# Kernel tuning notes

Measured on AMD Instinct MI355X. Metric: run time of the kernel, lower is better.

## Reference

```python
import jax, jax.numpy as jnp
import numpy as np

DIM = 256
HEADS = 8
PS = 8  # patch/window size
EPS = 1e-5


def _ln(x, g, b):
    m = x.mean(-1, keepdims=True)
    v = x.var(-1, keepdims=True)
    return (x - m) / jnp.sqrt(v + EPS) * g + b


def setup_inputs() -> dict:
    key = jax.random.key(0)
    ks = jax.random.split(key, 10)
    B, C, H, W = 4, DIM, 256, 256
    s = 0.02
    return {
        "y_lf": jax.random.normal(ks[0], (B, C, H, W), jnp.float32),
        "y_hf": jax.random.normal(ks[1], (B, C, H, W), jnp.float32),
        "g_lf": jnp.ones((C,), jnp.float32),
        "b_lf": jnp.zeros((C,), jnp.float32),
        "g_hf": jnp.ones((C,), jnp.float32),
        "b_hf": jnp.zeros((C,), jnp.float32),
        "Wq": jax.random.normal(ks[2], (C, C), jnp.float32) * s,
        "bq": jnp.zeros((C,), jnp.float32),
        "Wk": jax.random.normal(ks[3], (C, C), jnp.float32) * s,
        "bk": jnp.zeros((C,), jnp.float32),
        "Wv": jax.random.normal(ks[4], (C, C), jnp.float32) * s,
        "bv": jnp.zeros((C,), jnp.float32),
        "Wo": jax.random.normal(ks[5], (C, C), jnp.float32) * s,
        "bo": jnp.zeros((C,), jnp.float32),
    }


def reference(y_lf, y_hf, g_lf, b_lf, g_hf, b_hf, Wq, bq, Wk, bk, Wv, bv, Wo, bo):
    B, C, H, W = y_lf.shape
    ps = PS
    hd = C // HEADS
    nH, nW = H // ps, W // ps

    def win_tokens(x):
        # (B,C,H,W) -> (B*nH*nW, ps*ps, C)
        x = x.reshape(B, C, nH, ps, nW, ps)
        return x.transpose(0, 2, 4, 3, 5, 1).reshape(-1, ps * ps, C)

    lf = win_tokens(y_lf)
    hf = win_tokens(y_hf)  # residual + V source (un-normalized, as in torch code)

    q = _ln(lf, g_lf, b_lf) @ Wq.T + bq
    k = _ln(hf, g_hf, b_hf) @ Wk.T + bk
    v = hf @ Wv.T + bv

    BW, L, _ = q.shape
    q = q.reshape(BW, L, HEADS, hd)
    k = k.reshape(BW, L, HEADS, hd)
    v = v.reshape(BW, L, HEADS, hd)

    scale = 1.0 / np.sqrt(hd).astype(np.float32)
    scores = jnp.einsum('bqhd,bkhd->bhqk', q, k) * scale
    attn = jax.nn.softmax(scores, axis=-1)
    o = jnp.einsum('bhqk,bkhd->bqhd', attn, v).reshape(BW, L, C)
    o = o @ Wo.T + bo + hf  # out_proj + residual

    # window_reverse: (B*nH*nW, ps*ps, C) -> (B,C,H,W)
    o = o.reshape(B, nH, nW, ps, ps, C)
    o = o.transpose(0, 5, 1, 3, 2, 4).reshape(B, C, H, W)
    return o
```

## Files before the change

### kernel.cpp

```cpp
#include <hip/hip_runtime.h>

typedef float  f4     __attribute__((ext_vector_type(4)));
typedef float  f32x4  __attribute__((ext_vector_type(4)));
typedef short  short8 __attribute__((ext_vector_type(8)));
typedef __bf16 bf16x8 __attribute__((ext_vector_type(8)));
typedef int    int4v  __attribute__((ext_vector_type(4)));
typedef unsigned short us4 __attribute__((ext_vector_type(4)));

__device__ __forceinline__ unsigned short f2bf(float f) {
    unsigned int u = __builtin_bit_cast(unsigned int, f);
    u += 0x7FFFu + ((u >> 16) & 1u);
    return (unsigned short)(u >> 16);
}
__device__ __forceinline__ float bf2f(unsigned short h) {
    unsigned int u = ((unsigned int)h) << 16;
    return __builtin_bit_cast(float, u);
}
__device__ __forceinline__ f32x4 mfma_bf16(short8 a, short8 b, f32x4 c) {
    return __builtin_amdgcn_mfma_f32_16x16x32_bf16(
        __builtin_bit_cast(bf16x8, a), __builtin_bit_cast(bf16x8, b), c, 0, 0, 0);
}
__device__ __forceinline__ int cvt_pk_bf16(float lo, float hi) {
    int d;
    asm("v_cvt_pk_bf16_f32 %0, %1, %2" : "=v"(d) : "v"(lo), "v"(hi));
    return d;
}
__device__ __forceinline__ int bperm(int addr, int src) {
    return __builtin_amdgcn_ds_bpermute(addr, src);
}

__global__ void pcaf_precvt(const float* __restrict__ Wq, const float* __restrict__ bq,
                            const float* __restrict__ Wk, const float* __restrict__ bk,
                            const float* __restrict__ Wv, const float* __restrict__ Wo,
                            const float* __restrict__ g_lf, const float* __restrict__ b_lf,
                            const float* __restrict__ g_hf, const float* __restrict__ b_hf,
                            void* __restrict__ ws) {
    const int mat  = blockIdx.x >> 8;
    const int row  = blockIdx.x & 255;
    const int lane = threadIdx.x;
    const float* W = (mat == 0) ? Wq : (mat == 1) ? Wk : (mat == 2) ? Wv : Wo;
    f4 w = *(const f4*)(W + row * 256 + lane * 4);
    f4 wp = w;
    if (mat < 2) {
        const float* g = mat ? g_hf : g_lf;
        f4 gg = *(const f4*)(g + lane * 4);
        wp = w * gg;
    }
    us4 u;
    u[0] = f2bf(wp[0]); u[1] = f2bf(wp[1]); u[2] = f2bf(wp[2]); u[3] = f2bf(wp[3]);
    {
        const int ct   = row >> 4;
        const int l15r = row & 15;
        const int k_   = lane >> 3;
        const int g_   = (lane >> 1) & 3;
        const int e4   = (lane & 1) * 4;
        unsigned short* dst = (unsigned short*)ws + mat * 65536 +
                              (((ct * 8 + k_) * 64) + g_ * 16 + l15r) * 8 + e4;
        *(us4*)dst = u;
    }
    if (mat < 2) {
        const float* b = mat ? b_hf : b_lf;
        f4 bb = *(const f4*)(b + lane * 4);
        float rsum = wp[0] + wp[1] + wp[2] + wp[3];
        float cb   = bb[0] * w[0] + bb[1] * w[1] + bb[2] * w[2] + bb[3] * w[3];
        #pragma unroll
        for (int d = 1; d < 64; d <<= 1) {
            rsum += __shfl_xor(rsum, d);
            cb   += __shfl_xor(cb, d);
        }
        if (lane == 0) {
            float* cons = (float*)((char*)ws + 524288);
            cons[mat * 512 + 2 * row]     = rsum;
            cons[mat * 512 + 2 * row + 1] = cb + (mat ? bk[row] : bq[row]);
        }
    }
}

constexpr int RS  = 528;
constexpr int HWC = 65536;
constexpr int Wd  = 256;
constexpr int OA  = 0;
constexpr int OB  = 33792;
constexpr int OS  = 67584;

struct AccW { f32x4 a[4][2]; };
struct AccT { f32x4 a[2][4]; };

__device__ __forceinline__ AccW gemmW(const char* base,
                                      const unsigned short* __restrict__ Wbw,
                                      int lane, int g, int l15) {
    AccW r;
    f32x4 z = {0.f, 0.f, 0.f, 0.f};
    #pragma unroll
    for (int m = 0; m < 4; ++m) { r.a[m][0] = z; r.a[m][1] = z; }
    #pragma unroll
    for (int half = 0; half < 2; ++half) {
        short8 w0[4], w1[4];
        #pragma unroll
        for (int k = 0; k < 4; ++k) {
            w0[k] = *(const short8*)(Wbw + (half * 4 + k) * 512 + lane * 8);
            w1[k] = *(const short8*)(Wbw + 4096 + (half * 4 + k) * 512 + lane * 8);
        }
        #pragma unroll
        for (int k = 0; k < 4; ++k) {
            #pragma unroll
            for (int m = 0; m < 4; ++m) {
                short8 am = *(const short8*)(base + (16 * m + l15) * RS +
                                             ((half * 4 + k) * 32 + g * 8) * 2);
                r.a[m][0] = mfma_bf16(am, w0[k], r.a[m][0]);
                r.a[m][1] = mfma_bf16(am, w1[k], r.a[m][1]);
            }
        }
    }
    return r;
}

__device__ __forceinline__ AccT gemmWT(const char* base,
                                       const unsigned short* __restrict__ Wbw,
                                       int lane, int g, int l15) {
    AccT r;
    f32x4 z = {0.f, 0.f, 0.f, 0.f};
    #pragma unroll
    for (int n = 0; n < 4; ++n) { r.a[0][n] = z; r.a[1][n] = z; }
    #pragma unroll
    for (int half = 0; half < 2; ++half) {
        short8 w0[4], w1[4];
        #pragma unroll
        for (int k = 0; k < 4; ++k) {
            w0[k] = *(const short8*)(Wbw + (half * 4 + k) * 512 + lane * 8);
            w1[k] = *(const short8*)(Wbw + 4096 + (half * 4 + k) * 512 + lane * 8);
        }
        #pragma unroll
        for (int k = 0; k < 4; ++k) {
            #pragma unroll
            for (int n = 0; n < 4; ++n) {
                short8 tk = *(const short8*)(base + (16 * n + l15) * RS +
                                             ((half * 4 + k) * 32 + g * 8) * 2);
                r.a[0][n] = mfma_bf16(w0[k], tk, r.a[0][n]);
                r.a[1][n] = mfma_bf16(w1[k], tk, r.a[1][n]);
            }
        }
    }
    return r;
}

__device__ __forceinline__ short8 repack4(const int* p0, const int* p1,
                                          int a0, int a1, bool ghi) {
    int4v t;
    #pragma unroll
    for (int j = 0; j < 4; ++j) {
        int ad = (j >> 1) ? a1 : a0;
        int v0 = bperm(ad, p0[j & 1]);
        int v1 = bperm(ad, p1[j & 1]);
        t[j] = ghi ? v1 : v0;
    }
    return __builtin_bit_cast(short8, t);
}

__global__ __attribute__((amdgpu_flat_work_group_size(512, 512), amdgpu_waves_per_eu(2, 2)))
void pcaf14_kernel(
    const float* __restrict__ y_lf, const float* __restrict__ y_hf,
    const float* __restrict__ bv, const float* __restrict__ bo,
    const void* __restrict__ ws, float* __restrict__ out)
{
    __shared__ __align__(16) char sm[68608];

    const unsigned short* wsq = (const unsigned short*)ws;
    const unsigned short* wsk = wsq + 65536;
    const unsigned short* wsv = wsq + 131072;
    const unsigned short* wso = wsq + 196608;
    const float* qc = (const float*)((const char*)ws + 524288);
    const float* kc = qc + 512;

    const int tid = threadIdx.x;
    const int bid = blockIdx.x;
    const int wi  = ((bid & 7) << 9) | (bid >> 3);
    const int bb  = wi >> 10;
    const int nh  = (wi >> 5) & 31;
    const int nw  = wi & 31;
    const long win_base = (long)bb * 256 * HWC + (long)(nh * 8) * Wd + nw * 8;

    const int wave = tid >> 6;
    const int lane = tid & 63;
    const int g    = lane >> 4;
    const int l15  = lane & 15;
    const int c0   = 32 * wave + l15;

    {
        const int half = tid >> 8;
        const int t8   = tid & 255;
        const int pw4  = (t8 & 1) * 4;
        const int c2   = t8 >> 1;
        const float* src = half ? y_hf : y_lf;
        const int dst  = half ? OB : OA;
        const float* gp = src + win_base + (long)(2 * c2) * HWC + pw4;
        #pragma unroll
        for (int hh = 0; hh < 2; ++hh) {
            f4 v0[4], v1[4];
            #pragma unroll
            for (int p = 0; p < 4; ++p) {
                int ph = hh * 4 + p;
                v0[p] = *(const f4*)(gp + ph * Wd);
                v1[p] = *(const f4*)(gp + ph * Wd + HWC);
            }
            #pragma unroll
            for (int p = 0; p < 4; ++p) {
                int ph = hh * 4 + p;
                int tok0 = ph * 8 + pw4;
                #pragma unroll
                for (int j = 0; j < 4; ++j) {
                    unsigned int pk = (unsigned int)f2bf(v0[p][j]) |
                                      ((unsigned int)f2bf(v1[p][j]) << 16);
                    *(unsigned int*)(sm + dst + (tok0 + j) * RS + c2 * 4) = pk;
                }
            }
        }
    }
    __syncthreads();

    {
        const int t = tid >> 3, j = tid & 7;
        #pragma unroll
        for (int pass = 0; pass < 2; ++pass) {
            const int base = pass ? OB : OA;
            float sum = 0.f, ss = 0.f;
            #pragma unroll
            for (int r = 0; r < 4; ++r) {
                short8 raw = *(const short8*)(sm + base + t * RS + (j * 32 + r * 8) * 2);
                #pragma unroll
                for (int e = 0; e < 8; ++e) { float f = bf2f((unsigned short)raw[e]); sum += f; ss += f * f; }
            }
            sum += __shfl_xor(sum, 1); ss += __shfl_xor(ss, 1);
            sum += __shfl_xor(sum, 2); ss += __shfl_xor(ss, 2);
            sum += __shfl_xor(sum, 4); ss += __shfl_xor(ss, 4);
            float mean = sum * (1.f / 256.f);
            float rstd = rsqrtf(ss * (1.f / 256.f) - mean * mean + 1e-5f);
            if (j == 0) {
                float* S = (float*)(sm + OS);
                S[pass * 128 + t]      = mean;
                S[pass * 128 + 64 + t] = rstd;
            }
        }
    }
    __syncthreads();

    const float* S = (const float*)(sm + OS);
    const int  a0  = ((2 * (g & 1)) * 16 + l15) * 4;
    const int  a1  = a0 + 64;
    const bool ghi = (g >> 1) & 1;
    f32x4 z = {0.f, 0.f, 0.f, 0.f};

    short8 vf[2][2];
    {
        AccW vacc = gemmW(sm + OB, wsv + wave * 8192, lane, g, l15);
        float bv0 = bv[c0], bv1 = bv[c0 + 16];
        int vp[4][2][2];
        #pragma unroll
        for (int m = 0; m < 4; ++m) {
            vp[m][0][0] = cvt_pk_bf16(vacc.a[m][0][0] + bv0, vacc.a[m][0][1] + bv0);
            vp[m][0][1] = cvt_pk_bf16(vacc.a[m][0][2] + bv0, vacc.a[m][0][3] + bv0);
            vp[m][1][0] = cvt_pk_bf16(vacc.a[m][1][0] + bv1, vacc.a[m][1][1] + bv1);
            vp[m][1][1] = cvt_pk_bf16(vacc.a[m][1][2] + bv1, vacc.a[m][1][3] + bv1);
        }
        #pragma unroll
        for (int kk = 0; kk < 2; ++kk)
            #pragma unroll
            for (int n2 = 0; n2 < 2; ++n2)
                vf[kk][n2] = repack4(vp[2 * kk][n2], vp[2 * kk + 1][n2], a0, a1, ghi);
    }

    short8 kf[4];
    {
        AccT kacc = gemmWT(sm + OB, wsk + wave * 8192, lane, g, l15);
        float mh[4], rh[4];
        #pragma unroll
        for (int n = 0; n < 4; ++n) {
            mh[n] = S[128 + 16 * n + l15];
            rh[n] = S[192 + 16 * n + l15];
        }
        int kp[2][4][2];
        #pragma unroll
        for (int m = 0; m < 2; ++m) {
            int cb = 32 * wave + 16 * m + 4 * g;
            f4 c0v = *(const f4*)(kc + cb * 2);
            f4 c1v = *(const f4*)(kc + cb * 2 + 4);
            #pragma unroll
            for (int n = 0; n < 4; ++n) {
                float v0 = rh[n] * (kacc.a[m][n][0] - mh[n] * c0v[0]) + c0v[1];
                float v1 = rh[n] * (kacc.a[m][n][1] - mh[n] * c0v[2]) + c0v[3];
                float v2 = rh[n] * (kacc.a[m][n][2] - mh[n] * c1v[0]) + c1v[1];
                float v3 = rh[n] * (kacc.a[m][n][3] - mh[n] * c1v[2]) + c1v[3];
                kp[m][n][0] = cvt_pk_bf16(v0, v1);
                kp[m][n][1] = cvt_pk_bf16(v2, v3);
            }
        }
        #pragma unroll
        for (int x = 0; x < 4; ++x)
            kf[x] = repack4(kp[0][x], kp[1][x], a0, a1, ghi);
    }

    short8 qf[4];
    {
        AccT qacc = gemmWT(sm + OA, wsq + wave * 8192, lane, g, l15);
        const float SCALE = 0.17677669529663687f;
        float ml[4], rl[4];
        #pragma unroll
        for (int n = 0; n < 4; ++n) {
            ml[n] = S[16 * n + l15];
            rl[n] = S[64 + 16 * n + l15];
        }
        int qp[2][4][2];
        #pragma unroll
        for (int m = 0; m < 2; ++m) {
            int cb = 32 * wave + 16 * m + 4 * g;
            f4 c0v = *(const f4*)(qc + cb * 2);
            f4 c1v = *(const f4*)(qc + cb * 2 + 4);
            #pragma unroll
            for (int n = 0; n < 4; ++n) {
                float v0 = (rl[n] * (qacc.a[m][n][0] - ml[n] * c0v[0]) + c0v[1]) * SCALE;
                float v1 = (rl[n] * (qacc.a[m][n][1] - ml[n] * c0v[2]) + c0v[3]) * SCALE;
                float v2 = (rl[n] * (qacc.a[m][n][2] - ml[n] * c1v[0]) + c1v[1]) * SCALE;
                float v3 = (rl[n] * (qacc.a[m][n][3] - ml[n] * c1v[2]) + c1v[3]) * SCALE;
                qp[m][n][0] = cvt_pk_bf16(v0, v1);
                qp[m][n][1] = cvt_pk_bf16(v2, v3);
            }
        }
        #pragma unroll
        for (int x = 0; x < 4; ++x)
            qf[x] = repack4(qp[0][x], qp[1][x], a0, a1, ghi);
    }

    f32x4 o[4][2];
    {
        #pragma unroll
        for (int c = 0; c < 4; ++c) { o[c][0] = z; o[c][1] = z; }

        #pragma unroll
        for (int c = 0; c < 4; ++c) {
            f32x4 stc[4];
            #pragma unroll
            for (int nk = 0; nk < 4; ++nk)
                stc[nk] = mfma_bf16(kf[nk], qf[c], z);

            float mx = stc[0][0];
            #pragma unroll
            for (int nk = 0; nk < 4; ++nk)
                #pragma unroll
                for (int i = 0; i < 4; ++i) mx = fmaxf(mx, stc[nk][i]);
            mx = fmaxf(mx, __shfl_xor(mx, 16));
            mx = fmaxf(mx, __shfl_xor(mx, 32));
            float sum = 0.f;
            #pragma unroll
            for (int nk = 0; nk < 4; ++nk)
                #pragma unroll
                for (int i = 0; i < 4; ++i) {
                    float e = __expf(stc[nk][i] - mx);
                    stc[nk][i] = e;
                    sum += e;
                }
            sum += __shfl_xor(sum, 16);
            sum += __shfl_xor(sum, 32);
            float is = 1.f / sum;

            int pq[4][2];
            #pragma unroll
            for (int nk = 0; nk < 4; ++nk) {
                pq[nk][0] = cvt_pk_bf16(stc[nk][0] * is, stc[nk][1] * is);
                pq[nk][1] = cvt_pk_bf16(stc[nk][2] * is, stc[nk][3] * is);
            }

            #pragma unroll
            for (int kk = 0; kk < 2; ++kk) {
                short8 pf = repack4(pq[2 * kk], pq[2 * kk + 1], a0, a1, ghi);
                o[c][0] = mfma_bf16(pf, vf[kk][0], o[c][0]);
                o[c][1] = mfma_bf16(pf, vf[kk][1], o[c][1]);
            }
        }
    }
    __syncthreads();

    #pragma unroll
    for (int c = 0; c < 4; ++c)
        #pragma unroll
        for (int i = 0; i < 4; ++i) {
            int t = 16 * c + 4 * g + i;
            *(unsigned short*)(sm + OA + t * RS + c0 * 2)        = f2bf(o[c][0][i]);
            *(unsigned short*)(sm + OA + t * RS + (c0 + 16) * 2) = f2bf(o[c][1][i]);
        }
    __syncthreads();

    {
        AccW oacc = gemmW(sm + OA, wso + wave * 8192, lane, g, l15);
        float bo0 = bo[c0], bo1 = bo[c0 + 16];
        #pragma unroll
        for (int n = 0; n < 2; ++n) {
            float bon = n ? bo1 : bo0;
            int cout = c0 + 16 * n;
            #pragma unroll
            for (int m = 0; m < 4; ++m) {
                int tok0 = 16 * m + 4 * g;
                int ph = tok0 >> 3, pw = tok0 & 7;
                f4 ov;
                #pragma unroll
                for (int i = 0; i < 4; ++i) {
                    float rv = bf2f(*(const unsigned short*)(
                        sm + OB + (tok0 + i) * RS + cout * 2));
                    ov[i] = oacc.a[m][n][i] + bon + rv;
                }
                *(f4*)(out + win_base + (long)cout * HWC + ph * Wd + pw) = ov;
            }
        }
    }
}

extern "C" void kernel_launch(void* const* d_in, const int* in_sizes, int n_in,
                              void* d_out, int out_size, void* d_ws, size_t ws_size,
                              hipStream_t stream) {
    (void)in_sizes; (void)n_in; (void)out_size; (void)ws_size;
    const float* y_lf = (const float*)d_in[0];
    const float* y_hf = (const float*)d_in[1];
    const float* g_lf = (const float*)d_in[2];
    const float* b_lf = (const float*)d_in[3];
    const float* g_hf = (const float*)d_in[4];
    const float* b_hf = (const float*)d_in[5];
    const float* Wq   = (const float*)d_in[6];
    const float* bq   = (const float*)d_in[7];
    const float* Wk   = (const float*)d_in[8];
    const float* bk   = (const float*)d_in[9];
    const float* Wv   = (const float*)d_in[10];
    const float* bv   = (const float*)d_in[11];
    const float* Wo   = (const float*)d_in[12];
    const float* bo   = (const float*)d_in[13];
    float* out = (float*)d_out;

    pcaf_precvt<<<dim3(1024), dim3(64), 0, stream>>>(
        Wq, bq, Wk, bk, Wv, Wo, g_lf, b_lf, g_hf, b_hf, d_ws);
    pcaf14_kernel<<<dim3(4096), dim3(512), 0, stream>>>(
        y_lf, y_hf, bv, bo, d_ws, out);
}
```

Measured before the change: 418.5 us.

## Make attention kernel persistent and prefetch next window during output projection

Launches 256 persistent blocks that each loop over 16 windows instead of one block per window. The next window's global loads go into registers and are issued before the output-projection GEMM of the current window, so load latency overlaps compute. This removes per-block launch and fill overhead. In exchange it adds 16 f4 registers of prefetch state, extra barriers per iteration, and reduced parallelism, since 256 blocks may underfill the CUs at 2 waves per EU.

```diff
diff --git a/kernel.cpp b/kernel.cpp
--- a/kernel.cpp
+++ b/kernel.cpp
@@ -157,8 +157,19 @@
     return __builtin_bit_cast(short8, t);
 }
 
+__device__ __forceinline__ void prefetch_win(const float* __restrict__ src,
+                                             long win_base, int pw4, int c2,
+                                             f4* pre) {
+    const float* gp = src + win_base + (long)(2 * c2) * HWC + pw4;
+    #pragma unroll
+    for (int p = 0; p < 8; ++p) {
+        pre[p]     = *(const f4*)(gp + p * Wd);
+        pre[8 + p] = *(const f4*)(gp + p * Wd + HWC);
+    }
+}
+
 __global__ __attribute__((amdgpu_flat_work_group_size(512, 512), amdgpu_waves_per_eu(2, 2)))
-void pcaf14_kernel(
+void pcaf19_kernel(
     const float* __restrict__ y_lf, const float* __restrict__ y_hf,
     const float* __restrict__ bv, const float* __restrict__ bo,
     const void* __restrict__ ws, float* __restrict__ out)
@@ -173,12 +184,8 @@
     const float* kc = qc + 512;
 
     const int tid = threadIdx.x;
-    const int bid = blockIdx.x;
-    const int wi  = ((bid & 7) << 9) | (bid >> 3);
-    const int bb  = wi >> 10;
-    const int nh  = (wi >> 5) & 31;
-    const int nw  = wi & 31;
-    const long win_base = (long)bb * 256 * HWC + (long)(nh * 8) * Wd + nw * 8;
+    const int b   = blockIdx.x;
+    const int chunk = (b & 7) * 32 + (b >> 3);
 
     const int wave = tid >> 6;
     const int lane = tid & 63;
@@ -186,63 +193,12 @@
     const int l15  = lane & 15;
     const int c0   = 32 * wave + l15;
 
-    {
-        const int half = tid >> 8;
-        const int t8   = tid & 255;
-        const int pw4  = (t8 & 1) * 4;
-        const int c2   = t8 >> 1;
-        const float* src = half ? y_hf : y_lf;
-        const int dst  = half ? OB : OA;
-        const float* gp = src + win_base + (long)(2 * c2) * HWC + pw4;
-        #pragma unroll
-        for (int hh = 0; hh < 2; ++hh) {
-            f4 v0[4], v1[4];
-            #pragma unroll
-            for (int p = 0; p < 4; ++p) {
-                int ph = hh * 4 + p;
-                v0[p] = *(const f4*)(gp + ph * Wd);
-                v1[p] = *(const f4*)(gp + ph * Wd + HWC);
-            }
-            #pragma unroll
-            for (int p = 0; p < 4; ++p) {
-                int ph = hh * 4 + p;
-                int tok0 = ph * 8 + pw4;
-                #pragma unroll
-                for (int j = 0; j < 4; ++j) {
-                    unsigned int pk = (unsigned int)f2bf(v0[p][j]) |
-                                      ((unsigned int)f2bf(v1[p][j]) << 16);
-                    *(unsigned int*)(sm + dst + (tok0 + j) * RS + c2 * 4) = pk;
-                }
-            }
-        }
-    }
-    __syncthreads();
-
-    {
-        const int t = tid >> 3, j = tid & 7;
-        #pragma unroll
-        for (int pass = 0; pass < 2; ++pass) {
-            const int base = pass ? OB : OA;
-            float sum = 0.f, ss = 0.f;
-            #pragma unroll
-            for (int r = 0; r < 4; ++r) {
-                short8 raw = *(const short8*)(sm + base + t * RS + (j * 32 + r * 8) * 2);
-                #pragma unroll
-                for (int e = 0; e < 8; ++e) { float f = bf2f((unsigned short)raw[e]); sum += f; ss += f * f; }
-            }
-            sum += __shfl_xor(sum, 1); ss += __shfl_xor(ss, 1);
-            sum += __shfl_xor(sum, 2); ss += __shfl_xor(ss, 2);
-            sum += __shfl_xor(sum, 4); ss += __shfl_xor(ss, 4);
-            float mean = sum * (1.f / 256.f);
-            float rstd = rsqrtf(ss * (1.f / 256.f) - mean * mean + 1e-5f);
-            if (j == 0) {
-                float* S = (float*)(sm + OS);
-                S[pass * 128 + t]      = mean;
-                S[pass * 128 + 64 + t] = rstd;
-            }
-        }
-    }
-    __syncthreads();
+    const int phalf = tid >> 8;
+    const int t8    = tid & 255;
+    const int ppw4  = (t8 & 1) * 4;
+    const int pc2   = t8 >> 1;
+    const float* psrc = phalf ? y_hf : y_lf;
+    const int pdst  = phalf ? OB : OA;
 
     const float* S = (const float*)(sm + OS);
     const int  a0  = ((2 * (g & 1)) * 16 + l15) * 4;
@@ -250,88 +206,136 @@
     const bool ghi = (g >> 1) & 1;
     f32x4 z = {0.f, 0.f, 0.f, 0.f};
 
-    short8 vf[2][2];
-    {
-        AccW vacc = gemmW(sm + OB, wsv + wave * 8192, lane, g, l15);
-        float bv0 = bv[c0], bv1 = bv[c0 + 16];
-        int vp[4][2][2];
-        #pragma unroll
-        for (int m = 0; m < 4; ++m) {
-            vp[m][0][0] = cvt_pk_bf16(vacc.a[m][0][0] + bv0, vacc.a[m][0][1] + bv0);
-            vp[m][0][1] = cvt_pk_bf16(vacc.a[m][0][2] + bv0, vacc.a[m][0][3] + bv0);
-            vp[m][1][0] = cvt_pk_bf16(vacc.a[m][1][0] + bv1, vacc.a[m][1][1] + bv1);
-            vp[m][1][1] = cvt_pk_bf16(vacc.a[m][1][2] + bv1, vacc.a[m][1][3] + bv1);
-        }
-        #pragma unroll
-        for (int kk = 0; kk < 2; ++kk)
-            #pragma unroll
-            for (int n2 = 0; n2 < 2; ++n2)
-                vf[kk][n2] = repack4(vp[2 * kk][n2], vp[2 * kk + 1][n2], a0, a1, ghi);
-    }
-
-    short8 kf[4];
-    {
-        AccT kacc = gemmWT(sm + OB, wsk + wave * 8192, lane, g, l15);
-        float mh[4], rh[4];
-        #pragma unroll
-        for (int n = 0; n < 4; ++n) {
-            mh[n] = S[128 + 16 * n + l15];
-            rh[n] = S[192 + 16 * n + l15];
-        }
-        int kp[2][4][2];
-        #pragma unroll
-        for (int m = 0; m < 2; ++m) {
-            int cb = 32 * wave + 16 * m + 4 * g;
-            f4 c0v = *(const f4*)(kc + cb * 2);
-            f4 c1v = *(const f4*)(kc + cb * 2 + 4);
+    auto win_of = [&](int it) -> long {
+        int wi = chunk * 16 + it;
+        int bb = wi >> 10, nh = (wi >> 5) & 31, nw = wi & 31;
+        return (long)bb * 256 * HWC + (long)(nh * 8) * Wd + nw * 8;
+    };
+
+    f4 pre[16];
+    prefetch_win(psrc, win_of(0), ppw4, pc2, pre);
+
+    for (int it = 0; it < 16; ++it) {
+        const long win_base = win_of(it);
+
+        #pragma unroll
+        for (int p = 0; p < 8; ++p) {
+            int tok0 = p * 8 + ppw4;
+            #pragma unroll
+            for (int j = 0; j < 4; ++j) {
+                unsigned int pk = (unsigned int)cvt_pk_bf16(pre[p][j], pre[8 + p][j]);
+                *(unsigned int*)(sm + pdst + (tok0 + j) * RS + pc2 * 4) = pk;
+            }
+        }
+        __syncthreads();
+
+        {
+            const int t = tid >> 3, j = tid & 7;
+            #pragma unroll
+            for (int pass = 0; pass < 2; ++pass) {
+                const int base = pass ? OB : OA;
+                float sum = 0.f, ss = 0.f;
+                #pragma unroll
+                for (int r = 0; r < 4; ++r) {
+                    short8 raw = *(const short8*)(sm + base + t * RS + (j * 32 + r * 8) * 2);
+                    #pragma unroll
+                    for (int e = 0; e < 8; ++e) { float f = bf2f((unsigned short)raw[e]); sum += f; ss += f * f; }
+                }
+                sum += __shfl_xor(sum, 1); ss += __shfl_xor(ss, 1);
+                sum += __shfl_xor(sum, 2); ss += __shfl_xor(ss, 2);
+                sum += __shfl_xor(sum, 4); ss += __shfl_xor(ss, 4);
+                float mean = sum * (1.f / 256.f);
+                float rstd = rsqrtf(ss * (1.f / 256.f) - mean * mean + 1e-5f);
+                if (j == 0) {
+                    float* Sw = (float*)(sm + OS);
+                    Sw[pass * 128 + t]      = mean;
+                    Sw[pass * 128 + 64 + t] = rstd;
+                }
+            }
+        }
+        __syncthreads();
+
+        short8 vf[2][2];
+        {
+            AccW vacc = gemmW(sm + OB, wsv + wave * 8192, lane, g, l15);
+            float bv0 = bv[c0], bv1 = bv[c0 + 16];
+            int vp[4][2][2];
+            #pragma unroll
+            for (int m = 0; m < 4; ++m) {
+                vp[m][0][0] = cvt_pk_bf16(vacc.a[m][0][0] + bv0, vacc.a[m][0][1] + bv0);
+                vp[m][0][1] = cvt_pk_bf16(vacc.a[m][0][2] + bv0, vacc.a[m][0][3] + bv0);
+                vp[m][1][0] = cvt_pk_bf16(vacc.a[m][1][0] + bv1, vacc.a[m][1][1] + bv1);
+                vp[m][1][1] = cvt_pk_bf16(vacc.a[m][1][2] + bv1, vacc.a[m][1][3] + bv1);
+            }
+            #pragma unroll
+            for (int kk = 0; kk < 2; ++kk)
+                #pragma unroll
+                for (int n2 = 0; n2 < 2; ++n2)
+                    vf[kk][n2] = repack4(vp[2 * kk][n2], vp[2 * kk + 1][n2], a0, a1, ghi);
+        }
+
+        short8 kf[4];
+        {
+            AccT kacc = gemmWT(sm + OB, wsk + wave * 8192, lane, g, l15);
+            float mh[4], rh[4];
             #pragma unroll
             for (int n = 0; n < 4; ++n) {
-                float v0 = rh[n] * (kacc.a[m][n][0] - mh[n] * c0v[0]) + c0v[1];
-                float v1 = rh[n] * (kacc.a[m][n][1] - mh[n] * c0v[2]) + c0v[3];
-                float v2 = rh[n] * (kacc.a[m][n][2] - mh[n] * c1v[0]) + c1v[1];
-                float v3 = rh[n] * (kacc.a[m][n][3] - mh[n] * c1v[2]) + c1v[3];
-                kp[m][n][0] = cvt_pk_bf16(v0, v1);
-                kp[m][n][1] = cvt_pk_bf16(v2, v3);
-            }
-        }
-        #pragma unroll
-        for (int x = 0; x < 4; ++x)
-            kf[x] = repack4(kp[0][x], kp[1][x], a0, a1, ghi);
-    }
-
-    short8 qf[4];
-    {
-        AccT qacc = gemmWT(sm + OA, wsq + wave * 8192, lane, g, l15);
-        const float SCALE = 0.17677669529663687f;
-        float ml[4], rl[4];
-        #pragma unroll
-        for (int n = 0; n < 4; ++n) {
-            ml[n] = S[16 * n + l15];
-            rl[n] = S[64 + 16 * n + l15];
-        }
-        int qp[2][4][2];
-        #pragma unroll
-        for (int m = 0; m < 2; ++m) {
-            int cb = 32 * wave + 16 * m + 4 * g;
-            f4 c0v = *(const f4*)(qc + cb * 2);
-            f4 c1v = *(const f4*)(qc + cb * 2 + 4);
+                mh[n] = S[128 + 16 * n + l15];
+                rh[n] = S[192 + 16 * n + l15];
+            }
+            int kp[2][4][2];
+            #pragma unroll
+            for (int m = 0; m < 2; ++m) {
+                int cb = 32 * wave + 16 * m + 4 * g;
+                f4 c0v = *(const f4*)(kc + cb * 2);
+                f4 c1v = *(const f4*)(kc + cb * 2 + 4);
+                #pragma unroll
+                for (int n = 0; n < 4; ++n) {
+                    float v0 = rh[n] * (kacc.a[m][n][0] - mh[n] * c0v[0]) + c0v[1];
+                    float v1 = rh[n] * (kacc.a[m][n][1] - mh[n] * c0v[2]) + c0v[3];
+                    float v2 = rh[n] * (kacc.a[m][n][2] - mh[n] * c1v[0]) + c1v[1];
+                    float v3 = rh[n] * (kacc.a[m][n][3] - mh[n] * c1v[2]) + c1v[3];
+                    kp[m][n][0] = cvt_pk_bf16(v0, v1);
+                    kp[m][n][1] = cvt_pk_bf16(v2, v3);
+                }
+            }
+            #pragma unroll
+            for (int x = 0; x < 4; ++x)
+                kf[x] = repack4(kp[0][x], kp[1][x], a0, a1, ghi);
+        }
+
+        short8 qf[4];
+        {
+            AccT qacc = gemmWT(sm + OA, wsq + wave * 8192, lane, g, l15);
+            const float SCALE = 0.17677669529663687f;
+            float ml[4], rl[4];
             #pragma unroll
             for (int n = 0; n < 4; ++n) {
-                float v0 = (rl[n] * (qacc.a[m][n][0] - ml[n] * c0v[0]) + c0v[1]) * SCALE;
-                float v1 = (rl[n] * (qacc.a[m][n][1] - ml[n] * c0v[2]) + c0v[3]) * SCALE;
-                float v2 = (rl[n] * (qacc.a[m][n][2] - ml[n] * c1v[0]) + c1v[1]) * SCALE;
-                float v3 = (rl[n] * (qacc.a[m][n][3] - ml[n] * c1v[2]) + c1v[3]) * SCALE;
-                qp[m][n][0] = cvt_pk_bf16(v0, v1);
-                qp[m][n][1] = cvt_pk_bf16(v2, v3);
-            }
-        }
-        #pragma unroll
-        for (int x = 0; x < 4; ++x)
-            qf[x] = repack4(qp[0][x], qp[1][x], a0, a1, ghi);
-    }
-
-    f32x4 o[4][2];
-    {
+                ml[n] = S[16 * n + l15];
+                rl[n] = S[64 + 16 * n + l15];
+            }
+            int qp[2][4][2];
+            #pragma unroll
+            for (int m = 0; m < 2; ++m) {
+                int cb = 32 * wave + 16 * m + 4 * g;
+                f4 c0v = *(const f4*)(qc + cb * 2);
+                f4 c1v = *(const f4*)(qc + cb * 2 + 4);
+                #pragma unroll
+                for (int n = 0; n < 4; ++n) {
+                    float v0 = (rl[n] * (qacc.a[m][n][0] - ml[n] * c0v[0]) + c0v[1]) * SCALE;
+                    float v1 = (rl[n] * (qacc.a[m][n][1] - ml[n] * c0v[2]) + c0v[3]) * SCALE;
+                    float v2 = (rl[n] * (qacc.a[m][n][2] - ml[n] * c1v[0]) + c1v[1]) * SCALE;
+                    float v3 = (rl[n] * (qacc.a[m][n][3] - ml[n] * c1v[2]) + c1v[3]) * SCALE;
+                    qp[m][n][0] = cvt_pk_bf16(v0, v1);
+                    qp[m][n][1] = cvt_pk_bf16(v2, v3);
+                }
+            }
+            #pragma unroll
+            for (int x = 0; x < 4; ++x)
+                qf[x] = repack4(qp[0][x], qp[1][x], a0, a1, ghi);
+        }
+
+        f32x4 o[4][2];
         #pragma unroll
         for (int c = 0; c < 4; ++c) { o[c][0] = z; o[c][1] = z; }
 
@@ -376,40 +380,44 @@
                 o[c][1] = mfma_bf16(pf, vf[kk][1], o[c][1]);
             }
         }
-    }
-    __syncthreads();
-
-    #pragma unroll
-    for (int c = 0; c < 4; ++c)
-        #pragma unroll
-        for (int i = 0; i < 4; ++i) {
-            int t = 16 * c + 4 * g + i;
-            *(unsigned short*)(sm + OA + t * RS + c0 * 2)        = f2bf(o[c][0][i]);
-            *(unsigned short*)(sm + OA + t * RS + (c0 + 16) * 2) = f2bf(o[c][1][i]);
-        }
-    __syncthreads();
-
-    {
-        AccW oacc = gemmW(sm + OA, wso + wave * 8192, lane, g, l15);
-        float bo0 = bo[c0], bo1 = bo[c0 + 16];
-        #pragma unroll
-        for (int n = 0; n < 2; ++n) {
-            float bon = n ? bo1 : bo0;
-            int cout = c0 + 16 * n;
-            #pragma unroll
-            for (int m = 0; m < 4; ++m) {
-                int tok0 = 16 * m + 4 * g;
-                int ph = tok0 >> 3, pw = tok0 & 7;
-                f4 ov;
-                #pragma unroll
-                for (int i = 0; i < 4; ++i) {
-                    float rv = bf2f(*(const unsigned short*)(
-                        sm + OB + (tok0 + i) * RS + cout * 2));
-                    ov[i] = oacc.a[m][n][i] + bon + rv;
-                }
-                *(f4*)(out + win_base + (long)cout * HWC + ph * Wd + pw) = ov;
-            }
-        }
+        __syncthreads();
+
+        #pragma unroll
+        for (int c = 0; c < 4; ++c)
+            #pragma unroll
+            for (int i = 0; i < 4; ++i) {
+                int t = 16 * c + 4 * g + i;
+                *(unsigned short*)(sm + OA + t * RS + c0 * 2)        = f2bf(o[c][0][i]);
+                *(unsigned short*)(sm + OA + t * RS + (c0 + 16) * 2) = f2bf(o[c][1][i]);
+            }
+        __syncthreads();
+
+        if (it + 1 < 16)
+            prefetch_win(psrc, win_of(it + 1), ppw4, pc2, pre);
+
+        {
+            AccW oacc = gemmW(sm + OA, wso + wave * 8192, lane, g, l15);
+            float bo0 = bo[c0], bo1 = bo[c0 + 16];
+            #pragma unroll
+            for (int n = 0; n < 2; ++n) {
+                float bon = n ? bo1 : bo0;
+                int cout = c0 + 16 * n;
+                #pragma unroll
+                for (int m = 0; m < 4; ++m) {
+                    int tok0 = 16 * m + 4 * g;
+                    int ph = tok0 >> 3, pw = tok0 & 7;
+                    f4 ov;
+                    #pragma unroll
+                    for (int i = 0; i < 4; ++i) {
+                        float rv = bf2f(*(const unsigned short*)(
+                            sm + OB + (tok0 + i) * RS + cout * 2));
+                        ov[i] = oacc.a[m][n][i] + bon + rv;
+                    }
+                    *(f4*)(out + win_base + (long)cout * HWC + ph * Wd + pw) = ov;
+                }
+            }
+        }
+        __syncthreads();
     }
 }
 
@@ -435,6 +443,6 @@
 
     pcaf_precvt<<<dim3(1024), dim3(64), 0, stream>>>(
         Wq, bq, Wk, bk, Wv, Wo, g_lf, b_lf, g_hf, b_hf, d_ws);
-    pcaf14_kernel<<<dim3(4096), dim3(512), 0, stream>>>(
+    pcaf19_kernel<<<dim3(256), dim3(512), 0, stream>>>(
         y_lf, y_hf, bv, bo, d_ws, out);
 }
```

After: 926.5 us. +121.4%, slower.
